# Kernel optimization log

Hardware: AMD Instinct MI355X
Metric: run time of the kernel (lower is better)

The kernel has to match this reference:

```python
import jax, jax.numpy as jnp
import numpy as np
from jax import lax


def setup_inputs() -> dict:
    key = jax.random.key(0)
    ks = jax.random.split(key, 16)
    f32 = jnp.float32
    g = lambda k, shp, s=0.02: jax.random.normal(k, shp, dtype=f32) * s
    inp = {
        "x": jax.random.normal(ks[0], (4, 1, 4096), dtype=f32),
        # conv_time: Conv1d(1,128,3,pad=1)
        "conv_time_w": g(ks[1], (128, 1, 3)), "conv_time_b": jnp.zeros((128,), f32),
        "bn0_g": jnp.ones((128,), f32), "bn0_b": jnp.zeros((128,), f32),
        "bn0_m": jnp.zeros((128,), f32), "bn0_v": jnp.ones((128,), f32),
        # block1: Conv1d(128,256,3,pad=1)+BN
        "conv1_w": g(ks[2], (256, 128, 3)), "conv1_b": jnp.zeros((256,), f32),
        "bn1_g": jnp.ones((256,), f32), "bn1_b": jnp.zeros((256,), f32),
        "bn1_m": jnp.zeros((256,), f32), "bn1_v": jnp.ones((256,), f32),
        # block2: Conv1d(256,512,3,pad=1)+BN
        "conv2_w": g(ks[3], (512, 256, 3)), "conv2_b": jnp.zeros((512,), f32),
        "bn2_g": jnp.ones((512,), f32), "bn2_b": jnp.zeros((512,), f32),
        "bn2_m": jnp.zeros((512,), f32), "bn2_v": jnp.ones((512,), f32),
        # GAT 1: fc Linear(512,512), attn_fc Linear(1024,1)
        "gat1_fc_w": g(ks[4], (512, 512)), "gat1_fc_b": jnp.zeros((512,), f32),
        "gat1_attn_w": g(ks[5], (1024,)), "gat1_attn_b": jnp.zeros((), f32),
        # GAT 2: fc Linear(512,256), attn_fc Linear(512,1)
        "gat2_fc_w": g(ks[6], (256, 512)), "gat2_fc_b": jnp.zeros((256,), f32),
        "gat2_attn_w": g(ks[7], (512,)), "gat2_attn_b": jnp.zeros((), f32),
        # head: Linear(256,2)
        "fc_w": g(ks[8], (2, 256)), "fc_b": jnp.zeros((2,), f32),
    }
    return inp


def _conv1d(x, w, b):
    # x: [B,C,T], w: [O,C,3], padding=1
    y = lax.conv_general_dilated(x, w, window_strides=(1,), padding=((1, 1),),
                                 dimension_numbers=("NCH", "OIH", "NCH"))
    return y + b[None, :, None]


def _bn(x, g, b, m, v):
    # eval-mode BatchNorm1d over channel dim
    return (x - m[None, :, None]) * (g * lax.rsqrt(v + 1e-5))[None, :, None] + b[None, :, None]


def _maxpool2(x):
    return lax.reduce_window(x, -jnp.inf, lax.max, (1, 1, 2), (1, 1, 2), "VALID")


def _gat(x2d, fc_w, fc_b, aw, ab):
    # Faithful to: cat([h_i, h_j]) @ attn_w == h_i @ aw[:d] + h_j @ aw[d:]
    h = x2d @ fc_w.T + fc_b           # [N, d]
    d = h.shape[-1]
    s1 = h @ aw[:d]                   # [N] (query part, h.repeat(1,N))
    s2 = h @ aw[d:]                   # [N] (key part,   h.repeat(N,1))
    e = jax.nn.leaky_relu(s1[:, None] + s2[None, :] + ab, negative_slope=0.01)  # [N,N]
    att = jax.nn.softmax(e, axis=1)
    return att @ h                    # [N, d]


def reference(x, conv_time_w, conv_time_b, bn0_g, bn0_b, bn0_m, bn0_v,
              conv1_w, conv1_b, bn1_g, bn1_b, bn1_m, bn1_v,
              conv2_w, conv2_b, bn2_g, bn2_b, bn2_m, bn2_v,
              gat1_fc_w, gat1_fc_b, gat1_attn_w, gat1_attn_b,
              gat2_fc_w, gat2_fc_b, gat2_attn_w, gat2_attn_b,
              fc_w, fc_b):
    h = jax.nn.relu(_bn(_conv1d(x, conv_time_w, conv_time_b), bn0_g, bn0_b, bn0_m, bn0_v))
    h = _maxpool2(jax.nn.relu(_bn(_conv1d(h, conv1_w, conv1_b), bn1_g, bn1_b, bn1_m, bn1_v)))
    h = _maxpool2(jax.nn.relu(_bn(_conv1d(h, conv2_w, conv2_b), bn2_g, bn2_b, bn2_m, bn2_v)))
    h = jnp.transpose(h, (0, 2, 1))   # [B, S, 512]
    B, S, C = h.shape
    g = h.reshape(B * S, C)           # whole batch flattened into one graph (as in source)
    g = _gat(g, gat1_fc_w, gat1_fc_b, gat1_attn_w, gat1_attn_b)   # [N, 512]
    g = _gat(g, gat2_fc_w, gat2_fc_b, gat2_attn_w, gat2_attn_b)   # [N, 256]
    pooled = g.reshape(B, S, -1).mean(axis=1)                     # [B, 256]
    return pooled @ fc_w.T + fc_b     # [B, 2] (dropout is identity in eval)
```

## Files before the change

### kernel.cpp

```cpp
#include <hip/hip_runtime.h>
#include <hip/hip_bf16.h>
#include <math.h>


#define NN 4096
#define BB 4

__global__ void k_conv_time3(const float* __restrict__ x, const float* __restrict__ w,
                             const float* __restrict__ cb, const float* __restrict__ g,
                             const float* __restrict__ bbp, const float* __restrict__ m,
                             const float* __restrict__ v, float* __restrict__ out) {
  int gid = blockIdx.x * 256 + threadIdx.x;
  int t4 = gid & 1023;
  int o = (gid >> 10) & 127;
  int b = gid >> 17;
  int t = t4 * 4;
  float sc = g[o] * rsqrtf(v[o] + 1e-5f);
  float sh = (cb[o] - m[o]) * sc + bbp[o];
  const float* xb = x + b * 4096;
  float4 xc = *(const float4*)&xb[t];
  float xm = (t > 0) ? xb[t - 1] : 0.f;
  float xp = (t + 4 < 4096) ? xb[t + 4] : 0.f;
  const float* wo = w + o * 3;
  float w0 = wo[0], w1 = wo[1], w2 = wo[2];
  float4 y;
  y.x = fmaxf((w0 * xm   + w1 * xc.x + w2 * xc.y) * sc + sh, 0.f);
  y.y = fmaxf((w0 * xc.x + w1 * xc.y + w2 * xc.z) * sc + sh, 0.f);
  y.z = fmaxf((w0 * xc.y + w1 * xc.z + w2 * xc.w) * sc + sh, 0.f);
  y.w = fmaxf((w0 * xc.z + w1 * xc.w + w2 * xp  ) * sc + sh, 0.f);
  float* orow = out + ((size_t)(b * 128) + o) * 4104 + 4;
  *(float4*)&orow[t] = y;
  if (t4 == 0)    { orow[-4] = 0.f; orow[-3] = 0.f; orow[-2] = 0.f; orow[-1] = 0.f; }
  if (t4 == 1023) { orow[4096] = 0.f; orow[4097] = 0.f; orow[4098] = 0.f; orow[4099] = 0.f; }
}

template <int C, int TIN, int OPAD>
__global__ __launch_bounds__(64, 4)
void k_conv_fused2(const float* __restrict__ in, const float* __restrict__ w,
                   const float* __restrict__ cb, const float* __restrict__ g,
                   const float* __restrict__ bbp, const float* __restrict__ m,
                   const float* __restrict__ v, float* __restrict__ out, int OCH) {
  constexpr int TOUT = TIN / 2;
  constexpr int IST = TIN + 8;
  const int OST = TOUT + 2 * OPAD;
  int nT = TIN / 128;
  int bx = blockIdx.x;
  int tb = bx % nT;
  int oq = (bx / nT) % (OCH / 8);
  int b  = bx / (nT * (OCH / 8));
  int lane = threadIdx.x;
  int t0 = tb * 128;

  float acc[8][2];
  #pragma unroll
  for (int oi = 0; oi < 8; oi++) { acc[oi][0] = 0.f; acc[oi][1] = 0.f; }

  const float* wq = w + (size_t)(oq * 8) * C * 3;
  const float* xb = in + (size_t)(b * C) * IST + 4 + t0 + 2 * lane;

  float4 A = *(const float4*)(xb - 1);
  for (int cc = 0; cc < C; ++cc) {
    float4 An;
    if (cc + 1 < C) An = *(const float4*)(xb + (size_t)(cc + 1) * IST - 1);
    const float* wr = wq + (size_t)cc * 3;
    #pragma unroll
    for (int oi = 0; oi < 8; oi++) {
      const float* wo = wr + (size_t)oi * C * 3;
      float w0 = wo[0], w1 = wo[1], w2 = wo[2];
      acc[oi][0] += w0 * A.x + w1 * A.y + w2 * A.z;
      acc[oi][1] += w0 * A.y + w1 * A.z + w2 * A.w;
    }
    A = An;
  }

  int base_o = oq * 8;
  #pragma unroll
  for (int oi = 0; oi < 8; oi++) {
    int o = base_o + oi;
    float sc = g[o] * rsqrtf(v[o] + 1e-5f);
    float sh = (cb[o] - m[o]) * sc + bbp[o];
    float r = fmaxf(fmaxf(acc[oi][0] * sc + sh, acc[oi][1] * sc + sh), 0.f);
    out[((size_t)(b * OCH) + o) * OST + OPAD + tb * 64 + lane] = r;
  }
  if (OPAD > 0 && tb == 0) {
    if (lane < 8) {
      float* row = out + ((size_t)(b * OCH) + base_o + lane) * OST;
      row[0] = 0.f; row[1] = 0.f; row[2] = 0.f; row[3] = 0.f;
    } else if (lane < 16) {
      float* row = out + ((size_t)(b * OCH) + base_o + lane - 8) * OST;
      row[OPAD + TOUT + 0] = 0.f; row[OPAD + TOUT + 1] = 0.f;
      row[OPAD + TOUT + 2] = 0.f; row[OPAD + TOUT + 3] = 0.f;
    }
  }
}

__global__ __launch_bounds__(512, 4)
void k_gemm_chw(const float* __restrict__ A, const float* __restrict__ Wt,
                const float* __restrict__ bias, float* __restrict__ Cout) {
  constexpr int K = 512, N = 512;
  __shared__ float As[32][132];
  __shared__ float Bs[32][68];
  int i0 = blockIdx.x * 128, j0 = blockIdx.y * 64;
  int tid = threadIdx.x;
  int tx = tid & 15, ty = tid >> 4;
  int b = i0 >> 10, s0 = i0 & 1023;
  const float* Ab = A + (size_t)b * K * 1024 + s0;

  float acc[4][4];
  #pragma unroll
  for (int ii = 0; ii < 4; ii++)
    #pragma unroll
    for (int jj = 0; jj < 4; jj++) acc[ii][jj] = 0.f;

  int ka = (tid + 0) >> 5, i4a = tid & 31;
  int kb = (tid + 512) >> 5, i4b = tid & 31;
  float4 pa0, pa1; float pb[4];

  pa0 = *(const float4*)&Ab[(size_t)ka * 1024 + 4 * i4a];
  pa1 = *(const float4*)&Ab[(size_t)kb * 1024 + 4 * i4b];
  #pragma unroll
  for (int r = 0; r < 4; r++) {
    int e = tid + 512 * r; int j = e >> 5, k = e & 31;
    pb[r] = Wt[(size_t)(j0 + j) * K + k];
  }

  for (int kt = 0; kt < K; kt += 32) {
    *(float4*)&As[ka][4 * i4a] = pa0;
    *(float4*)&As[kb][4 * i4b] = pa1;
    #pragma unroll
    for (int r = 0; r < 4; r++) {
      int e = tid + 512 * r; int j = e >> 5, k = e & 31;
      Bs[k][j] = pb[r];
    }
    __syncthreads();
    int ktn = (kt + 32 < K) ? kt + 32 : 0;
    float4 na0 = *(const float4*)&Ab[(size_t)(ktn + ka) * 1024 + 4 * i4a];
    float4 na1 = *(const float4*)&Ab[(size_t)(ktn + kb) * 1024 + 4 * i4b];
    float nb[4];
    #pragma unroll
    for (int r = 0; r < 4; r++) {
      int e = tid + 512 * r; int j = e >> 5, k = e & 31;
      nb[r] = Wt[(size_t)(j0 + j) * K + ktn + k];
    }
    #pragma unroll 4
    for (int kk = 0; kk < 32; ++kk) {
      float4 a4 = *(const float4*)&As[kk][ty * 4];
      float4 b4 = *(const float4*)&Bs[kk][tx * 4];
      float a[4] = {a4.x, a4.y, a4.z, a4.w};
      float bv[4] = {b4.x, b4.y, b4.z, b4.w};
      #pragma unroll
      for (int ii = 0; ii < 4; ii++)
        #pragma unroll
        for (int jj = 0; jj < 4; jj++) acc[ii][jj] += a[ii] * bv[jj];
    }
    __syncthreads();
    pa0 = na0; pa1 = na1;
    #pragma unroll
    for (int r = 0; r < 4; r++) pb[r] = nb[r];
  }

  float4 bias4 = *(const float4*)&bias[j0 + 4 * tx];
  #pragma unroll
  for (int ii = 0; ii < 4; ii++) {
    int i = i0 + ty * 4 + ii;
    float4 o4;
    o4.x = acc[ii][0] + bias4.x; o4.y = acc[ii][1] + bias4.y;
    o4.z = acc[ii][2] + bias4.z; o4.w = acc[ii][3] + bias4.w;
    *(float4*)&Cout[(size_t)i * N + j0 + 4 * tx] = o4;
  }
}

__global__ __launch_bounds__(256, 4)
void k_gemm_rm(const float* __restrict__ A, const float* __restrict__ Wt,
               const float* __restrict__ bias, float* __restrict__ Cout) {
  constexpr int K = 512, N = 256;
  __shared__ float As[32][68];
  __shared__ float Bs[32][68];
  int i0 = blockIdx.x * 64, j0 = blockIdx.y * 64;
  int tid = threadIdx.x;
  int tx = tid & 15, ty = tid >> 4;

  float acc[4][4];
  #pragma unroll
  for (int ii = 0; ii < 4; ii++)
    #pragma unroll
    for (int jj = 0; jj < 4; jj++) acc[ii][jj] = 0.f;

  float4 pa[2]; float pb[8];
  #pragma unroll
  for (int r = 0; r < 2; r++) {
    int e4 = tid + 256 * r; int i = e4 >> 3, k4 = e4 & 7;
    pa[r] = *(const float4*)&A[(size_t)(i0 + i) * K + 4 * k4];
  }
  #pragma unroll
  for (int r = 0; r < 8; r++) {
    int e = tid + 256 * r; int j = e >> 5, k = e & 31;
    pb[r] = Wt[(size_t)(j0 + j) * K + k];
  }

  for (int kt = 0; kt < K; kt += 32) {
    #pragma unroll
    for (int r = 0; r < 2; r++) {
      int e4 = tid + 256 * r; int i = e4 >> 3, k4 = e4 & 7;
      As[4 * k4 + 0][i] = pa[r].x; As[4 * k4 + 1][i] = pa[r].y;
      As[4 * k4 + 2][i] = pa[r].z; As[4 * k4 + 3][i] = pa[r].w;
    }
    #pragma unroll
    for (int r = 0; r < 8; r++) {
      int e = tid + 256 * r; int j = e >> 5, k = e & 31;
      Bs[k][j] = pb[r];
    }
    __syncthreads();
    int ktn = (kt + 32 < K) ? kt + 32 : 0;
    float4 na[2]; float nb[8];
    #pragma unroll
    for (int r = 0; r < 2; r++) {
      int e4 = tid + 256 * r; int i = e4 >> 3, k4 = e4 & 7;
      na[r] = *(const float4*)&A[(size_t)(i0 + i) * K + ktn + 4 * k4];
    }
    #pragma unroll
    for (int r = 0; r < 8; r++) {
      int e = tid + 256 * r; int j = e >> 5, k = e & 31;
      nb[r] = Wt[(size_t)(j0 + j) * K + ktn + k];
    }
    #pragma unroll 4
    for (int kk = 0; kk < 32; ++kk) {
      float4 a4 = *(const float4*)&As[kk][ty * 4];
      float4 b4 = *(const float4*)&Bs[kk][tx * 4];
      float a[4] = {a4.x, a4.y, a4.z, a4.w};
      float bv[4] = {b4.x, b4.y, b4.z, b4.w};
      #pragma unroll
      for (int ii = 0; ii < 4; ii++)
        #pragma unroll
        for (int jj = 0; jj < 4; jj++) acc[ii][jj] += a[ii] * bv[jj];
    }
    __syncthreads();
    pa[0] = na[0]; pa[1] = na[1];
    #pragma unroll
    for (int r = 0; r < 8; r++) pb[r] = nb[r];
  }

  float4 bias4 = *(const float4*)&bias[j0 + 4 * tx];
  #pragma unroll
  for (int ii = 0; ii < 4; ii++) {
    int i = i0 + ty * 4 + ii;
    float4 o4;
    o4.x = acc[ii][0] + bias4.x; o4.y = acc[ii][1] + bias4.y;
    o4.z = acc[ii][2] + bias4.z; o4.w = acc[ii][3] + bias4.w;
    *(float4*)&Cout[(size_t)i * N + j0 + 4 * tx] = o4;
  }
}

template <int D>
__global__ void k_rowdot(const float* __restrict__ h, const float* __restrict__ aw,
                         float* __restrict__ s1, float* __restrict__ s2,
                         int* __restrict__ rnk) {
  if (blockIdx.x < 16) rnk[blockIdx.x * 256 + threadIdx.x] = 0;
  int wid = threadIdx.x >> 6, lane = threadIdx.x & 63;
  int i = blockIdx.x * 4 + wid;
  const float* hr = h + (size_t)i * D;
  float d1 = 0.f, d2 = 0.f;
  #pragma unroll
  for (int d = lane; d < D; d += 64) {
    float hv = hr[d];
    d1 += hv * aw[d];
    d2 += hv * aw[D + d];
  }
  for (int off = 32; off; off >>= 1) {
    d1 += __shfl_down(d1, off, 64);
    d2 += __shfl_down(d2, off, 64);
  }
  if (lane == 0) { s1[i] = d1; s2[i] = d2; }
}

__global__ void k_rank(const float* __restrict__ s2v, int* __restrict__ rnk) {
  __shared__ float ls[1024];
  int j = blockIdx.x * 256 + threadIdx.x;
  int base = blockIdx.y * 1024;
  float vj = s2v[j];
  for (int e = threadIdx.x; e < 1024; e += 256) ls[e] = s2v[base + e];
  __syncthreads();
  int cnt = 0;
  #pragma unroll 8
  for (int r = 0; r < 1024; ++r) {
    float vr = ls[r];
    cnt += (vr < vj || (vr == vj && (base + r) < j)) ? 1 : 0;
  }
  atomicAdd(&rnk[j], cnt);
}

__global__ void k_scatter(const float* __restrict__ s2v, const int* __restrict__ rnk,
                          float* __restrict__ svals, int* __restrict__ sidx) {
  int j = blockIdx.x * 256 + threadIdx.x;
  int r = rnk[j];
  svals[r] = s2v[j];
  sidx[r] = j;
}

__global__ void k_tw(const float* __restrict__ s1, const float* __restrict__ svals,
                     const float* __restrict__ abp, int* __restrict__ tarr,
                     float* __restrict__ Aarr, float* __restrict__ Barr,
                     float* __restrict__ wp, float* __restrict__ wm) {
  int i = blockIdx.x * 256 + threadIdx.x;
  float ab = abp[0], M2 = svals[NN - 1];
  float alpha = s1[i] + ab;
  float cthr = -alpha;
  int lo = 0, hi = NN;
  while (lo < hi) {
    int mid = (lo + hi) >> 1;
    if (svals[mid] < cthr) lo = mid + 1; else hi = mid;
  }
  tarr[i] = lo;
  float e1 = alpha + M2;
  float gam = fmaxf(e1, 0.01f * e1);
  Aarr[i] = expf(e1 - gam);
  Barr[i] = expf(0.01f * e1 - gam);
  float d = svals[i] - M2;
  wp[i] = expf(d);
  wm[i] = expf(0.01f * d);
}

__global__ void k_scan_den(const float* __restrict__ wp, const float* __restrict__ wm,
                           float* __restrict__ preden, float* __restrict__ sufden) {
  __shared__ float csP[256], csM[256];
  int tid = threadIdx.x;
  int base = tid * 16;
  float sm = 0.f, sp = 0.f;
  for (int u = 0; u < 16; u++) { sm += wm[base + u]; sp += wp[base + u]; }
  csM[tid] = sm; csP[tid] = sp;
  __syncthreads();
  float offM = 0.f;
  for (int c = 0; c < tid; c++) offM += csM[c];
  float offP = 0.f;
  for (int c = tid + 1; c < 256; c++) offP += csP[c];
  float run = offM;
  for (int u = 0; u < 16; u++) { preden[base + u] = run; run += wm[base + u]; }
  if (tid == 255) preden[NN] = run;
  float runp = offP;
  if (tid == 255) sufden[NN] = 0.f;
  for (int u = 15; u >= 0; u--) { runp += wp[base + u]; sufden[base + u] = runp; }
}

template <int D>
__global__ void k_chunksum(const float* __restrict__ h, const int* __restrict__ sidx,
                           const float* __restrict__ wp, const float* __restrict__ wm,
                           float* __restrict__ csP, float* __restrict__ csM) {
  constexpr int CPT = D / 256;
  int c = blockIdx.x, tid = threadIdx.x;
  __shared__ int lidx[32];
  __shared__ float lwp[32], lwm[32];
  if (tid < 32) {
    int r = c * 32 + tid;
    lidx[tid] = sidx[r]; lwp[tid] = wp[r]; lwm[tid] = wm[r];
  }
  __syncthreads();
  float aP[CPT], aM[CPT];
  #pragma unroll
  for (int q = 0; q < CPT; q++) { aP[q] = 0.f; aM[q] = 0.f; }
  for (int u = 0; u < 32; u++) {
    const float* hr = h + (size_t)lidx[u] * D;
    float fp = lwp[u], fm = lwm[u];
    #pragma unroll
    for (int q = 0; q < CPT; q++) {
      float hv = hr[tid + q * 256];
      aP[q] += fp * hv; aM[q] += fm * hv;
    }
  }
  #pragma unroll
  for (int q = 0; q < CPT; q++) {
    csP[(size_t)c * D + tid + q * 256] = aP[q];
    csM[(size_t)c * D + tid + q * 256] = aM[q];
  }
}

template <int D>
__global__ void k_chunkoff(const float* __restrict__ csP, const float* __restrict__ csM,
                           float* __restrict__ offP, float* __restrict__ offM) {
  int d = blockIdx.x * 256 + threadIdx.x;
  float rm = 0.f;
  for (int cb = 0; cb < 128; cb += 16) {
    float vals[16];
    #pragma unroll
    for (int u = 0; u < 16; u++) vals[u] = csM[(size_t)(cb + u) * D + d];
    #pragma unroll
    for (int u = 0; u < 16; u++) { offM[(size_t)(cb + u) * D + d] = rm; rm += vals[u]; }
  }
  float rp = 0.f;
  for (int cb = 127; cb >= 15; cb -= 16) {
    float vals[16];
    #pragma unroll
    for (int u = 0; u < 16; u++) vals[u] = csP[(size_t)(cb - u) * D + d];
    #pragma unroll
    for (int u = 0; u < 16; u++) { offP[(size_t)(cb - u) * D + d] = rp; rp += vals[u]; }
  }
}

template <int D>
__global__ void k_scanwrite(const float* __restrict__ h, const int* __restrict__ sidx,
                            const float* __restrict__ wp, const float* __restrict__ wm,
                            const float* __restrict__ offP, const float* __restrict__ offM,
                            float* __restrict__ Pre, float* __restrict__ Suf) {
  constexpr int CPT = D / 256;
  int c = blockIdx.x, tid = threadIdx.x;
  __shared__ int lidx[32];
  __shared__ float lwp[32], lwm[32];
  if (tid < 32) {
    int r = c * 32 + tid;
    lidx[tid] = sidx[r]; lwp[tid] = wp[r]; lwm[tid] = wm[r];
  }
  __syncthreads();
  float runM[CPT], runP[CPT];
  #pragma unroll
  for (int q = 0; q < CPT; q++) {
    int d = tid + q * 256;
    runM[q] = offM[(size_t)c * D + d];
    runP[q] = offP[(size_t)c * D + d];
  }
  for (int u = 0; u < 32; u++) {
    const float* hr = h + (size_t)lidx[u] * D;
    float fm = lwm[u];
    #pragma unroll
    for (int q = 0; q < CPT; q++) {
      int d = tid + q * 256;
      Pre[(size_t)(c * 32 + u) * D + d] = runM[q];
      runM[q] += fm * hr[d];
    }
  }
  if (c == 127) {
    #pragma unroll
    for (int q = 0; q < CPT; q++) Pre[(size_t)NN * D + tid + q * 256] = runM[q];
    #pragma unroll
    for (int q = 0; q < CPT; q++) Suf[(size_t)NN * D + tid + q * 256] = 0.f;
  }
  for (int u = 31; u >= 0; u--) {
    const float* hr = h + (size_t)lidx[u] * D;
    float fp = lwp[u];
    #pragma unroll
    for (int q = 0; q < CPT; q++) {
      int d = tid + q * 256;
      runP[q] += fp * hr[d];
      Suf[(size_t)(c * 32 + u) * D + d] = runP[q];
    }
  }
}

template <int D>
__global__ void k_apply(const float* __restrict__ Pre, const float* __restrict__ Suf,
                        const float* __restrict__ preden, const float* __restrict__ sufden,
                        const int* __restrict__ tarr, const float* __restrict__ Aarr,
                        const float* __restrict__ Barr, float* __restrict__ outg) {
  int i = blockIdx.x;
  int t = tarr[i];
  float A = Aarr[i], Bv = Barr[i];
  float den = A * sufden[t] + Bv * preden[t];
  float inv = 1.f / den;
  const float* Pr = Pre + (size_t)t * D;
  const float* Sr = Suf + (size_t)t * D;
  for (int d = threadIdx.x; d < D; d += 256)
    outg[(size_t)i * D + d] = (A * Sr[d] + Bv * Pr[d]) * inv;
}

__global__ void k_pool(const float* __restrict__ g2, float* __restrict__ pp) {
  int b = blockIdx.x >> 4, ch = blockIdx.x & 15;
  const float* base = g2 + ((size_t)(b * 1024) + ch * 64) * 256 + threadIdx.x;
  float s = 0.f;
  for (int r = 0; r < 64; r++) s += base[(size_t)r * 256];
  pp[(size_t)blockIdx.x * 256 + threadIdx.x] = s;
}

__global__ void k_head2(const float* __restrict__ pp, const float* __restrict__ fcw,
                        const float* __restrict__ fcb, float* __restrict__ out) {
  __shared__ float pooled[4][256];
  int tid = threadIdx.x;
  for (int b = 0; b < 4; b++) {
    float s = 0.f;
    for (int ch = 0; ch < 16; ch++) s += pp[(size_t)(b * 16 + ch) * 256 + tid];
    pooled[b][tid] = s * (1.f / 1024.f);
  }
  __syncthreads();
  if (tid < 8) {
    int b = tid >> 1, c = tid & 1;
    float acc = fcb[c];
    for (int cc = 0; cc < 256; cc++) acc += pooled[b][cc] * fcw[c * 256 + cc];
    out[b * 2 + c] = acc;
  }
}

extern "C" void kernel_launch(void* const* d_in, const int* in_sizes, int n_in,
                              void* d_out, int out_size, void* d_ws, size_t ws_size,
                              hipStream_t stream) {
  const float* x    = (const float*)d_in[0];
  const float* ctw  = (const float*)d_in[1];
  const float* ctb  = (const float*)d_in[2];
  const float* bn0g = (const float*)d_in[3];
  const float* bn0b = (const float*)d_in[4];
  const float* bn0m = (const float*)d_in[5];
  const float* bn0v = (const float*)d_in[6];
  const float* c1w  = (const float*)d_in[7];
  const float* c1b  = (const float*)d_in[8];
  const float* bn1g = (const float*)d_in[9];
  const float* bn1b = (const float*)d_in[10];
  const float* bn1m = (const float*)d_in[11];
  const float* bn1v = (const float*)d_in[12];
  const float* c2w  = (const float*)d_in[13];
  const float* c2b  = (const float*)d_in[14];
  const float* bn2g = (const float*)d_in[15];
  const float* bn2b = (const float*)d_in[16];
  const float* bn2m = (const float*)d_in[17];
  const float* bn2v = (const float*)d_in[18];
  const float* g1w  = (const float*)d_in[19];
  const float* g1b  = (const float*)d_in[20];
  const float* g1aw = (const float*)d_in[21];
  const float* g1ab = (const float*)d_in[22];
  const float* g2w  = (const float*)d_in[23];
  const float* g2b  = (const float*)d_in[24];
  const float* g2aw = (const float*)d_in[25];
  const float* g2ab = (const float*)d_in[26];
  const float* fcw  = (const float*)d_in[27];
  const float* fcb  = (const float*)d_in[28];
  float* ws = (float*)d_ws;

  const size_t S0SZ = (size_t)4 * 128 * 4104;
  const size_t S1SZ = (size_t)4 * 256 * 2056;
  const size_t SLOT = (size_t)(NN + 1) * 512;
  float* slot0 = ws;
  float* slot1 = ws + S0SZ;
  float* slot2 = slot1 + S1SZ;
  float* slot3 = slot2 + SLOT;
  float* sm    = slot3 + SLOT;
  float* s1    = sm;
  float* s2    = sm + 4096;
  float* svals = sm + 8192;
  int*   sidx  = (int*)(sm + 12288);
  int*   tarr  = (int*)(sm + 16384);
  float* Aarr  = sm + 20480;
  float* Barr  = sm + 24576;
  float* wp    = sm + 28672;
  float* wm    = sm + 32768;
  float* preden = sm + 36864;
  float* sufden = sm + 40968;
  float* csP   = sm + 45072;
  float* csM   = csP + 65536;
  float* offP  = csM + 65536;
  float* offM  = offP + 65536;
  int*   rnk   = (int*)(offM + 65536);
  float* pp    = offM + 65536 + 4096;

  k_conv_time3<<<BB * 128 * 1024 / 256, 256, 0, stream>>>(x, ctw, ctb, bn0g, bn0b, bn0m, bn0v, slot0);
  k_conv_fused2<128, 4096, 4><<<BB * 32 * 32, 64, 0, stream>>>(
      slot0, c1w, c1b, bn1g, bn1b, bn1m, bn1v, slot1, 256);
  k_conv_fused2<256, 2048, 0><<<BB * 64 * 16, 64, 0, stream>>>(
      slot1, c2w, c2b, bn2g, bn2b, bn2m, bn2v, slot2, 512);

  k_gemm_chw<<<dim3(32, 8), 512, 0, stream>>>(slot2, g1w, g1b, slot3);
  k_rowdot<512><<<NN / 4, 256, 0, stream>>>(slot3, g1aw, s1, s2, rnk);
  k_rank<<<dim3(16, 4), 256, 0, stream>>>(s2, rnk);
  k_scatter<<<16, 256, 0, stream>>>(s2, rnk, svals, sidx);
  k_tw<<<NN / 256, 256, 0, stream>>>(s1, svals, g1ab, tarr, Aarr, Barr, wp, wm);
  k_scan_den<<<1, 256, 0, stream>>>(wp, wm, preden, sufden);
  k_chunksum<512><<<128, 256, 0, stream>>>(slot3, sidx, wp, wm, csP, csM);
  k_chunkoff<512><<<2, 256, 0, stream>>>(csP, csM, offP, offM);
  k_scanwrite<512><<<128, 256, 0, stream>>>(slot3, sidx, wp, wm, offP, offM, slot1, slot0);
  k_apply<512><<<NN, 256, 0, stream>>>(slot1, slot0, preden, sufden, tarr, Aarr, Barr, slot2);

  k_gemm_rm<<<dim3(64, 4), 256, 0, stream>>>(slot2, g2w, g2b, slot3);
  k_rowdot<256><<<NN / 4, 256, 0, stream>>>(slot3, g2aw, s1, s2, rnk);
  k_rank<<<dim3(16, 4), 256, 0, stream>>>(s2, rnk);
  k_scatter<<<16, 256, 0, stream>>>(s2, rnk, svals, sidx);
  k_tw<<<NN / 256, 256, 0, stream>>>(s1, svals, g2ab, tarr, Aarr, Barr, wp, wm);
  k_scan_den<<<1, 256, 0, stream>>>(wp, wm, preden, sufden);
  k_chunksum<256><<<128, 256, 0, stream>>>(slot3, sidx, wp, wm, csP, csM);
  k_chunkoff<256><<<1, 256, 0, stream>>>(csP, csM, offP, offM);
  k_scanwrite<256><<<128, 256, 0, stream>>>(slot3, sidx, wp, wm, offP, offM, slot1, slot0);
  k_apply<256><<<NN, 256, 0, stream>>>(slot1, slot0, preden, sufden, tarr, Aarr, Barr, slot2);

  k_pool<<<BB * 16, 256, 0, stream>>>(slot2, pp);
  k_head2<<<1, 256, 0, stream>>>(pp, fcw, fcb, (float*)d_out);
}
```

Measured before the change: 450.6 us.

## Rework conv kernels to 4 timesteps per lane with shuffle halo exchange

The fused conv+BN+ReLU+maxpool kernel now has each lane load an aligned float4 of 4 input timesteps and produce 2 pooled outputs for 4 output channels, instead of 2 inputs for 8 channels. Neighbour halo contributions are accumulated as partial sums and passed between lanes with shuffles, with the block edges handled by scalar loads. This raises input reuse per load, keeps loads aligned and doubles the grid's channel groups. The trade-off is more weight loads per input and extra shuffle work.

```diff
diff --git a/kernel.cpp b/kernel.cpp
--- a/kernel.cpp
+++ b/kernel.cpp
@@ -36,58 +36,78 @@
 
 template <int C, int TIN, int OPAD>
 __global__ __launch_bounds__(64, 4)
-void k_conv_fused2(const float* __restrict__ in, const float* __restrict__ w,
+void k_conv_fused4(const float* __restrict__ in, const float* __restrict__ w,
                    const float* __restrict__ cb, const float* __restrict__ g,
                    const float* __restrict__ bbp, const float* __restrict__ m,
                    const float* __restrict__ v, float* __restrict__ out, int OCH) {
   constexpr int TOUT = TIN / 2;
   constexpr int IST = TIN + 8;
   const int OST = TOUT + 2 * OPAD;
-  int nT = TIN / 128;
+  int nT = TIN / 256;
   int bx = blockIdx.x;
   int tb = bx % nT;
-  int oq = (bx / nT) % (OCH / 8);
-  int b  = bx / (nT * (OCH / 8));
+  int oq = (bx / nT) % (OCH / 4);
+  int b  = bx / (nT * (OCH / 4));
   int lane = threadIdx.x;
-  int t0 = tb * 128;
-
-  float acc[8][2];
-  #pragma unroll
-  for (int oi = 0; oi < 8; oi++) { acc[oi][0] = 0.f; acc[oi][1] = 0.f; }
-
-  const float* wq = w + (size_t)(oq * 8) * C * 3;
-  const float* xb = in + (size_t)(b * C) * IST + 4 + t0 + 2 * lane;
-
-  float4 A = *(const float4*)(xb - 1);
+  int t0 = tb * 256;
+
+  float A1[4], A2[4], A3[4], A4[4], E[4], F[4], GE[4], GF[4];
+  #pragma unroll
+  for (int oi = 0; oi < 4; oi++) {
+    A1[oi] = A2[oi] = A3[oi] = A4[oi] = 0.f;
+    E[oi] = F[oi] = GE[oi] = GF[oi] = 0.f;
+  }
+
+  const float* wq = w + (size_t)(oq * 4) * C * 3;
+  const float* rowb = in + (size_t)(b * C) * IST;
+  const float* xb = rowb + 4 + t0 + 4 * lane;
+
+  float4 X = *(const float4*)xb;
   for (int cc = 0; cc < C; ++cc) {
-    float4 An;
-    if (cc + 1 < C) An = *(const float4*)(xb + (size_t)(cc + 1) * IST - 1);
+    float4 Xn;
+    if (cc + 1 < C) Xn = *(const float4*)(xb + (size_t)(cc + 1) * IST);
+    float xmL = rowb[(size_t)cc * IST + 3 + t0];
+    float xpR = rowb[(size_t)cc * IST + 4 + t0 + 256];
     const float* wr = wq + (size_t)cc * 3;
     #pragma unroll
-    for (int oi = 0; oi < 8; oi++) {
+    for (int oi = 0; oi < 4; oi++) {
       const float* wo = wr + (size_t)oi * C * 3;
       float w0 = wo[0], w1 = wo[1], w2 = wo[2];
-      acc[oi][0] += w0 * A.x + w1 * A.y + w2 * A.z;
-      acc[oi][1] += w0 * A.y + w1 * A.z + w2 * A.w;
-    }
-    A = An;
-  }
-
-  int base_o = oq * 8;
-  #pragma unroll
-  for (int oi = 0; oi < 8; oi++) {
+      A1[oi] += w1 * X.x + w2 * X.y;
+      A2[oi] += w0 * X.x + w1 * X.y + w2 * X.z;
+      A3[oi] += w0 * X.y + w1 * X.z + w2 * X.w;
+      A4[oi] += w0 * X.z + w1 * X.w;
+      E[oi]  += w0 * X.w;
+      F[oi]  += w2 * X.x;
+      GE[oi] += w0 * xmL;
+      GF[oi] += w2 * xpR;
+    }
+    X = Xn;
+  }
+
+  int base_o = oq * 4;
+  #pragma unroll
+  for (int oi = 0; oi < 4; oi++) {
     int o = base_o + oi;
     float sc = g[o] * rsqrtf(v[o] + 1e-5f);
     float sh = (cb[o] - m[o]) * sc + bbp[o];
-    float r = fmaxf(fmaxf(acc[oi][0] * sc + sh, acc[oi][1] * sc + sh), 0.f);
-    out[((size_t)(b * OCH) + o) * OST + OPAD + tb * 64 + lane] = r;
+    float eIn = __shfl_up(E[oi], 1, 64);
+    if (lane == 0) eIn = GE[oi];
+    float fIn = __shfl_down(F[oi], 1, 64);
+    if (lane == 63) fIn = GF[oi];
+    float y0 = A1[oi] + eIn;
+    float y3 = A4[oi] + fIn;
+    float2 r;
+    r.x = fmaxf(fmaxf(y0 * sc + sh, A2[oi] * sc + sh), 0.f);
+    r.y = fmaxf(fmaxf(A3[oi] * sc + sh, y3 * sc + sh), 0.f);
+    *(float2*)&out[((size_t)(b * OCH) + o) * OST + OPAD + tb * 128 + 2 * lane] = r;
   }
   if (OPAD > 0 && tb == 0) {
-    if (lane < 8) {
+    if (lane < 4) {
       float* row = out + ((size_t)(b * OCH) + base_o + lane) * OST;
       row[0] = 0.f; row[1] = 0.f; row[2] = 0.f; row[3] = 0.f;
-    } else if (lane < 16) {
-      float* row = out + ((size_t)(b * OCH) + base_o + lane - 8) * OST;
+    } else if (lane < 8) {
+      float* row = out + ((size_t)(b * OCH) + base_o + lane - 4) * OST;
       row[OPAD + TOUT + 0] = 0.f; row[OPAD + TOUT + 1] = 0.f;
       row[OPAD + TOUT + 2] = 0.f; row[OPAD + TOUT + 3] = 0.f;
     }
@@ -547,9 +567,9 @@
   float* pp    = offM + 65536 + 4096;
 
   k_conv_time3<<<BB * 128 * 1024 / 256, 256, 0, stream>>>(x, ctw, ctb, bn0g, bn0b, bn0m, bn0v, slot0);
-  k_conv_fused2<128, 4096, 4><<<BB * 32 * 32, 64, 0, stream>>>(
+  k_conv_fused4<128, 4096, 4><<<BB * 16 * 64, 64, 0, stream>>>(
       slot0, c1w, c1b, bn1g, bn1b, bn1m, bn1v, slot1, 256);
-  k_conv_fused2<256, 2048, 0><<<BB * 64 * 16, 64, 0, stream>>>(
+  k_conv_fused4<256, 2048, 0><<<BB * 8 * 128, 64, 0, stream>>>(
       slot1, c2w, c2b, bn2g, bn2b, bn2m, bn2v, slot2, 512);
 
   k_gemm_chw<<<dim3(32, 8), 512, 0, stream>>>(slot2, g1w, g1b, slot3);
```

New measurement: 462.6 us. 2.7% more time.
